# Performance work log

Measured on AMD Instinct MI355X. Metric: run time of the kernel, lower is better.

Reference implementation:

```python
import jax, jax.numpy as jnp
import numpy as np

B, N, E = 2, 20000, 160000
D, U = 1, 100          # input_dim, num_units
IN = D + U             # 101
NEG_SLOPE = 0.2        # PyG GATv2Conv default


def setup_inputs() -> dict:
    key = jax.random.key(0)
    ks = jax.random.split(key, 20)
    s = 0.1
    inp = {
        "inputs": jax.random.normal(ks[0], (B, N * D), jnp.float32),
        "state": jax.random.normal(ks[1], (B, N * U), jnp.float32),
        "src": jax.random.randint(ks[2], (E,), 0, N),
        "dst": jax.random.randint(ks[3], (E,), 0, N),
        # GATv2Conv(101, 200) params: lin_l, lin_r, att, out-bias
        "Wl1": jax.random.normal(ks[4], (IN, 2 * U), jnp.float32) * s,
        "bl1": jax.random.normal(ks[5], (2 * U,), jnp.float32) * s,
        "Wr1": jax.random.normal(ks[6], (IN, 2 * U), jnp.float32) * s,
        "br1": jax.random.normal(ks[7], (2 * U,), jnp.float32) * s,
        "att1": jax.random.normal(ks[8], (2 * U,), jnp.float32) * s,
        "bg1": jax.random.normal(ks[9], (2 * U,), jnp.float32) * s,
        "bias0": jax.random.normal(ks[10], (2 * U,), jnp.float32) * s,
        # GATv2Conv(101, 100) params
        "Wl2": jax.random.normal(ks[11], (IN, U), jnp.float32) * s,
        "bl2": jax.random.normal(ks[12], (U,), jnp.float32) * s,
        "Wr2": jax.random.normal(ks[13], (IN, U), jnp.float32) * s,
        "br2": jax.random.normal(ks[14], (U,), jnp.float32) * s,
        "att2": jax.random.normal(ks[15], (U,), jnp.float32) * s,
        "bg2": jax.random.normal(ks[16], (U,), jnp.float32) * s,
        "bias1": jax.random.normal(ks[17], (U,), jnp.float32) * s,
    }
    return inp


def _gatv2(x, src_f, dst_f, Wl, bl, Wr, br, att, bg):
    # x: (B, N, IN); edges (with self-loops) flow src -> dst.
    xl = x @ Wl + bl                                   # (B, N, C) source transform
    xr = x @ Wr + br                                   # (B, N, C) target transform
    msg = jax.nn.leaky_relu(xl[:, src_f] + xr[:, dst_f], NEG_SLOPE)  # (B, Ef, C)
    e = jnp.einsum('bec,c->be', msg, att)              # (B, Ef) attention logits
    seg_max = jax.vmap(lambda v: jax.ops.segment_max(v, dst_f, num_segments=N))(e)
    ea = jnp.exp(e - seg_max[:, dst_f])
    denom = jax.vmap(lambda v: jax.ops.segment_sum(v, dst_f, num_segments=N))(ea)
    alpha = ea / denom[:, dst_f]                       # per-target softmax
    out = jax.vmap(
        lambda a, xs: jax.ops.segment_sum(a[:, None] * xs, dst_f, num_segments=N)
    )(alpha, xl[:, src_f])                             # (B, N, C)
    return out + bg


def reference(inputs, state, src, dst,
              Wl1, bl1, Wr1, br1, att1, bg1, bias0,
              Wl2, bl2, Wr2, br2, att2, bg2, bias1):
    loops = jnp.arange(N)
    src_f = jnp.concatenate([src, loops])              # PyG adds self-loops
    dst_f = jnp.concatenate([dst, loops])
    inputs3 = inputs.reshape(B, N, D)
    state3 = state.reshape(B, N, U)

    # _gc1: GATv2(101 -> 200) + bias_0, sigmoid gates r, u
    xs = jnp.concatenate([inputs3, state3], axis=2)    # (B, N, 101)
    g1 = _gatv2(xs, src_f, dst_f, Wl1, bl1, Wr1, br1, att1, bg1) + bias0
    val = jax.nn.sigmoid(g1)                           # (B, N, 200)
    r = val[..., :U].reshape(B, N * U)
    u = val[..., U:].reshape(B, N * U)

    # _gc2: GATv2(101 -> 100) on [inputs, r*state] + bias_1, tanh
    xs2 = jnp.concatenate([inputs3, (r * state).reshape(B, N, U)], axis=2)
    c = jnp.tanh(_gatv2(xs2, src_f, dst_f, Wl2, bl2, Wr2, br2, att2, bg2) + bias1)
    c = c.reshape(B, N * U)

    new_state = u * state + (1.0 - u) * c              # (B, N*U)
    return new_state
```

## Files before the change

kernel.cpp:

```cpp
#include <hip/hip_runtime.h>
#include <stdint.h>

typedef __attribute__((ext_vector_type(8))) short short8;
typedef __attribute__((ext_vector_type(4))) short short4v;
typedef __attribute__((ext_vector_type(4))) float f32x4;

static constexpr int BB = 2, NN = 20000, UU = 100;
static constexpr int C1 = 200, C2 = 100;
static constexpr int MT = BB * NN;
static constexpr int MPAD = 40064;
static constexpr float NEG = 0.2f;

__device__ __forceinline__ float b2f(short s) {
  union { uint32_t u; float f; } cv; cv.u = ((uint32_t)(uint16_t)s) << 16; return cv.f;
}
__device__ __forceinline__ short f2b(float x) {
  union { float f; uint32_t u; } cv; cv.f = x;
  uint32_t r = cv.u + 0x7FFFu + ((cv.u >> 16) & 1u);
  return (short)(r >> 16);
}

#define GL2LDS(gsrc, ldst)                                                          \
  __builtin_amdgcn_global_load_lds((const __attribute__((address_space(1))) void*)(gsrc), \
                                   (__attribute__((address_space(3))) void*)(ldst), 16, 0, 0)


__global__ void k_prep(const float* __restrict__ inp, const float* __restrict__ st,
                       const float* __restrict__ Wl1, const float* __restrict__ Wr1,
                       const float* __restrict__ Wl2, const float* __restrict__ Wr2,
                       short* __restrict__ A, short* __restrict__ BT1,
                       short* __restrict__ BT2, int* __restrict__ cursor) {
  int t = blockIdx.x * 256 + threadIdx.x;
  if (t < MT * 16) {
    int r = t >> 4, g = t & 15;
    short8 v;
#pragma unroll
    for (int j = 0; j < 8; ++j) {
      int e = g * 8 + j;
      float x = 0.f;
      if (e == 0) x = inp[r];
      else if (e <= 100) x = st[(size_t)r * 100 + e - 1];
      v[j] = f2b(x);
    }
    *(short8*)(A + (size_t)r * 128 + ((g ^ (r & 7)) << 3)) = v;
  }
  if (t < 512 * 16) {
    int n = t >> 4, g = t & 15;
    short8 v;
#pragma unroll
    for (int j = 0; j < 8; ++j) {
      int k = g * 8 + j;
      float x = 0.f;
      if (k < 101 && n < 400)
        x = (n < 200) ? Wl1[(size_t)k * 200 + n] : Wr1[(size_t)k * 200 + n - 200];
      v[j] = f2b(x);
    }
    *(short8*)(BT1 + (size_t)n * 128 + ((g ^ (n & 7)) << 3)) = v;
  }
  if (t < 256 * 16) {
    int n = t >> 4, g = t & 15;
    short8 v;
#pragma unroll
    for (int j = 0; j < 8; ++j) {
      int k = g * 8 + j;
      int ksrc = (k < 100) ? k + 1 : ((k == 100) ? 0 : -1);
      float x = 0.f;
      if (ksrc >= 0 && n < 200)
        x = (n < 100) ? Wl2[(size_t)ksrc * 100 + n] : Wr2[(size_t)ksrc * 100 + n - 100];
      v[j] = f2b(x);
    }
    *(short8*)(BT2 + (size_t)n * 128 + ((g ^ (n & 7)) << 3)) = v;
  }
  if (t < NN) cursor[t] = 0;
}


__global__ void k_hist(const int* __restrict__ dst, int E, int* __restrict__ hist) {
  int e = blockIdx.x * 256 + threadIdx.x;
  if (e < E) atomicAdd(&hist[dst[e]], 1);
}

__global__ __launch_bounds__(1024) void k_scan(int* __restrict__ histcur,
                                               int* __restrict__ rowptr, int N, int E) {
  __shared__ int part[1024];
  int t = threadIdx.x;
  int CH = (N + 1023) / 1024;
  int beg = t * CH; if (beg > N) beg = N;
  int end = beg + CH; if (end > N) end = N;
  int s = 0;
  for (int i = beg; i < end; ++i) s += histcur[i];
  part[t] = s;
  __syncthreads();
  for (int off = 1; off < 1024; off <<= 1) {
    int v = (t >= off) ? part[t - off] : 0;
    __syncthreads();
    part[t] += v;
    __syncthreads();
  }
  int base = (t == 0) ? 0 : part[t - 1];
  for (int i = beg; i < end; ++i) {
    int h = histcur[i];
    rowptr[i] = base;
    histcur[i] = base;
    base += h;
  }
  if (t == 1023) rowptr[N] = part[1023];
}

__global__ void k_scatter(const int* __restrict__ src, const int* __restrict__ dst, int E,
                          int* __restrict__ cursor, int* __restrict__ col) {
  int e = blockIdx.x * 256 + threadIdx.x;
  if (e < E) {
    int p = atomicAdd(&cursor[dst[e]], 1);
    col[p] = src[e];
  }
}


template<int NOUT, int SPLIT>
__global__ __launch_bounds__(256) void k_gemm(
    const short* __restrict__ A, const short* __restrict__ BT,
    const float* __restrict__ bias_l, const float* __restrict__ bias_r,
    short* __restrict__ X) {
  __shared__ __align__(16) short As[128 * 128];
  __shared__ __align__(16) short Bs[128 * 128];
  int tid = threadIdx.x;
  int m0 = blockIdx.x * 128;
  int n0 = blockIdx.y * 128;
  {
    const short* gA = A + (size_t)m0 * 128;
    const short* gB = BT + (size_t)n0 * 128;
#pragma unroll
    for (int i = 0; i < 8; ++i) {
      GL2LDS(gA + i * 2048 + tid * 8, As + i * 2048 + tid * 8);
      GL2LDS(gB + i * 2048 + tid * 8, Bs + i * 2048 + tid * 8);
    }
  }
  __syncthreads();

  int wv = tid >> 6, lane = tid & 63;
  int m_off = (wv & 1) * 64, n_off = (wv >> 1) * 64;
  int lrow = lane & 15, lk = lane >> 4;
  f32x4 acc[4][4];
#pragma unroll
  for (int i = 0; i < 4; ++i)
#pragma unroll
    for (int j = 0; j < 4; ++j) acc[i][j] = (f32x4){0.f, 0.f, 0.f, 0.f};

#pragma unroll
  for (int kk = 0; kk < 4; ++kk) {
    int g = kk * 4 + lk;
    short8 a[4], b[4];
#pragma unroll
    for (int f = 0; f < 4; ++f) {
      int ra = m_off + f * 16 + lrow;
      a[f] = *(const short8*)(As + ra * 128 + ((g ^ (ra & 7)) << 3));
      int rb = n_off + f * 16 + lrow;
      b[f] = *(const short8*)(Bs + rb * 128 + ((g ^ (rb & 7)) << 3));
    }
#pragma unroll
    for (int i = 0; i < 4; ++i)
#pragma unroll
      for (int j = 0; j < 4; ++j)
        acc[i][j] = __builtin_amdgcn_mfma_f32_16x16x32_bf16(a[i], b[j], acc[i][j], 0, 0, 0);
  }

#pragma unroll
  for (int j = 0; j < 4; ++j) {
    int nc = n0 + n_off + j * 16 + lrow;
    bool nok = nc < NOUT;
    float bv = 0.f;
    int coff = 0;
    if (nok) {
      bv   = (nc < SPLIT) ? bias_l[nc] : bias_r[nc - SPLIT];
      coff = (nc < SPLIT) ? nc : 2 * SPLIT + (nc - SPLIT);
    }
#pragma unroll
    for (int i = 0; i < 4; ++i) {
      int mb = m0 + m_off + i * 16 + lk * 4;
#pragma unroll
      for (int r = 0; r < 4; ++r) {
        int m = mb + r;
        if (nok && m < MT) {
          int b_   = (m >= NN) ? 1 : 0;
          int node = m - b_ * NN;
          X[(size_t)node * (4 * SPLIT) + coff + b_ * SPLIT] = f2b(acc[i][j][r] + bv);
        }
      }
    }
  }
}


__global__ __launch_bounds__(256) void k_agg1(
    const short* __restrict__ X1, const int* __restrict__ rowptr, const int* __restrict__ col,
    const float* __restrict__ att, const float* __restrict__ bgv, const float* __restrict__ bias0,
    const float* __restrict__ st, const float* __restrict__ inp,
    short* __restrict__ A2, float* __restrict__ uu) {
  int w = threadIdx.x >> 6, lane = threadIdx.x & 63;
  int n = blockIdx.x * 4 + w;
  if (n >= NN) return;
  int half = lane >> 5, ll = lane & 31;
  int c0 = (ll < 25 ? ll : 24) * 8;
  int idx = half * NN + n;
  const short* xb = X1 + (size_t)half * 200 + c0;

  float attv[8], xrv[8], num[8];
  {
    f32x4 a0 = (f32x4){0,0,0,0}, a1 = (f32x4){0,0,0,0};
    if (ll < 25) { a0 = *(const f32x4*)(att + c0); a1 = *(const f32x4*)(att + c0 + 4); }
#pragma unroll
    for (int q = 0; q < 4; ++q) { attv[q] = a0[q]; attv[4 + q] = a1[q]; }
    short8 xr8 = *(const short8*)(X1 + (size_t)n * 800 + 400 + half * 200 + c0);
#pragma unroll
    for (int q = 0; q < 8; ++q) xrv[q] = (ll < 25) ? b2f(xr8[q]) : 0.f;
  }
  float denom;
  {
    short8 v = *(const short8*)(xb + (size_t)n * 800);
    float xs[8], e = 0.f;
#pragma unroll
    for (int q = 0; q < 8; ++q) {
      xs[q] = b2f(v[q]);
      float msg = xs[q] + xrv[q];
      msg = (msg > 0.f) ? msg : NEG * msg;
      e = fmaf(msg, attv[q], e);
    }
#pragma unroll
    for (int off = 16; off > 0; off >>= 1) e += __shfl_xor(e, off);
    float pe = __expf(e);
    denom = pe;
#pragma unroll
    for (int q = 0; q < 8; ++q) num[q] = pe * xs[q];
  }

  int beg = rowptr[n], end = rowptr[n + 1];
  for (int bp = beg; bp < end; bp += 64) {
    int cnt = min(end - bp, 64);
    int cv = col[bp + (lane < cnt ? lane : 0)];
    int p = 0;
    for (; p + 4 <= cnt; p += 4) {
      int s0 = __shfl(cv, p), s1 = __shfl(cv, p + 1);
      int s2 = __shfl(cv, p + 2), s3 = __shfl(cv, p + 3);
      short8 v0 = *(const short8*)(xb + (size_t)s0 * 800);
      short8 v1 = *(const short8*)(xb + (size_t)s1 * 800);
      short8 v2 = *(const short8*)(xb + (size_t)s2 * 800);
      short8 v3 = *(const short8*)(xb + (size_t)s3 * 800);
      float xs0[8], xs1[8], xs2[8], xs3[8];
      float e0 = 0.f, e1 = 0.f, e2 = 0.f, e3 = 0.f;
#pragma unroll
      for (int q = 0; q < 8; ++q) {
        float m_;
        xs0[q] = b2f(v0[q]); m_ = xs0[q] + xrv[q]; m_ = (m_ > 0.f) ? m_ : NEG * m_; e0 = fmaf(m_, attv[q], e0);
        xs1[q] = b2f(v1[q]); m_ = xs1[q] + xrv[q]; m_ = (m_ > 0.f) ? m_ : NEG * m_; e1 = fmaf(m_, attv[q], e1);
        xs2[q] = b2f(v2[q]); m_ = xs2[q] + xrv[q]; m_ = (m_ > 0.f) ? m_ : NEG * m_; e2 = fmaf(m_, attv[q], e2);
        xs3[q] = b2f(v3[q]); m_ = xs3[q] + xrv[q]; m_ = (m_ > 0.f) ? m_ : NEG * m_; e3 = fmaf(m_, attv[q], e3);
      }
#pragma unroll
      for (int off = 16; off > 0; off >>= 1) {
        e0 += __shfl_xor(e0, off);
        e1 += __shfl_xor(e1, off);
        e2 += __shfl_xor(e2, off);
        e3 += __shfl_xor(e3, off);
      }
      float pe0 = __expf(e0), pe1 = __expf(e1), pe2 = __expf(e2), pe3 = __expf(e3);
      denom += (pe0 + pe1) + (pe2 + pe3);
#pragma unroll
      for (int q = 0; q < 8; ++q)
        num[q] = fmaf(pe3, xs3[q], fmaf(pe2, xs2[q], fmaf(pe1, xs1[q], fmaf(pe0, xs0[q], num[q]))));
    }
    for (; p < cnt; ++p) {
      int s0 = __shfl(cv, p);
      short8 v0 = *(const short8*)(xb + (size_t)s0 * 800);
      float xs0[8], e0 = 0.f;
#pragma unroll
      for (int q = 0; q < 8; ++q) {
        xs0[q] = b2f(v0[q]);
        float m_ = xs0[q] + xrv[q]; m_ = (m_ > 0.f) ? m_ : NEG * m_;
        e0 = fmaf(m_, attv[q], e0);
      }
#pragma unroll
      for (int off = 16; off > 0; off >>= 1) e0 += __shfl_xor(e0, off);
      float pe0 = __expf(e0);
      denom += pe0;
#pragma unroll
      for (int q = 0; q < 8; ++q) num[q] = fmaf(pe0, xs0[q], num[q]);
    }
  }

  float invd = 1.f / denom;
  if (ll < 25) {
    f32x4 g0 = *(const f32x4*)(bgv + c0),   g1 = *(const f32x4*)(bgv + c0 + 4);
    f32x4 h0 = *(const f32x4*)(bias0 + c0), h1 = *(const f32x4*)(bias0 + c0 + 4);
    float vq[8];
#pragma unroll
    for (int q = 0; q < 4; ++q) {
      float o0 = fmaf(num[q], invd, g0[q] + h0[q]);
      vq[q] = 1.f / (1.f + __expf(-o0));
      float o1 = fmaf(num[4 + q], invd, g1[q] + h1[q]);
      vq[4 + q] = 1.f / (1.f + __expf(-o1));
    }
    size_t sb = (size_t)idx * UU;
    if (ll < 12) {
      f32x4 s0 = *(const f32x4*)(st + sb + c0), s1 = *(const f32x4*)(st + sb + c0 + 4);
      short8 wv;
#pragma unroll
      for (int q = 0; q < 4; ++q) { wv[q] = f2b(vq[q] * s0[q]); wv[4 + q] = f2b(vq[4 + q] * s1[q]); }
      *(short8*)(A2 + (size_t)idx * 128 + ((ll ^ (idx & 7)) << 3)) = wv;
    } else if (ll == 12) {
      f32x4 s0 = *(const f32x4*)(st + sb + 96);
      short8 wv;
#pragma unroll
      for (int q = 0; q < 4; ++q) wv[q] = f2b(vq[q] * s0[q]);
      wv[4] = f2b(inp[idx]); wv[5] = 0; wv[6] = 0; wv[7] = 0;
      *(short8*)(A2 + (size_t)idx * 128 + ((12 ^ (idx & 7)) << 3)) = wv;
      *(f32x4*)(uu + sb) = (f32x4){vq[4], vq[5], vq[6], vq[7]};
    } else {
      int uo = c0 - 100;
      *(f32x4*)(uu + sb + uo)     = (f32x4){vq[0], vq[1], vq[2], vq[3]};
      *(f32x4*)(uu + sb + uo + 4) = (f32x4){vq[4], vq[5], vq[6], vq[7]};
      if (ll < 16) {
        short8 z = (short8){0,0,0,0,0,0,0,0};
        *(short8*)(A2 + (size_t)idx * 128 + ((ll ^ (idx & 7)) << 3)) = z;
      }
    }
  }
}

__global__ __launch_bounds__(256) void k_agg2(
    const short* __restrict__ X2, const int* __restrict__ rowptr, const int* __restrict__ col,
    const float* __restrict__ att, const float* __restrict__ bgv, const float* __restrict__ bias1,
    const float* __restrict__ st, float* __restrict__ out) {
  int w = threadIdx.x >> 6, lane = threadIdx.x & 63;
  int n = blockIdx.x * 4 + w;
  if (n >= NN) return;
  int half = lane >> 5, ll = lane & 31;
  int c0 = (ll < 25 ? ll : 24) * 4;
  int idx = half * NN + n;
  const short* xb = X2 + (size_t)half * 100 + c0;

  float attv[4], xrv[4], num[4];
  {
    f32x4 a0 = (f32x4){0,0,0,0};
    if (ll < 25) a0 = *(const f32x4*)(att + c0);
#pragma unroll
    for (int q = 0; q < 4; ++q) attv[q] = a0[q];
    short4v xr4 = *(const short4v*)(X2 + (size_t)n * 400 + 200 + half * 100 + c0);
#pragma unroll
    for (int q = 0; q < 4; ++q) xrv[q] = (ll < 25) ? b2f(xr4[q]) : 0.f;
  }
  float denom;
  {
    short4v v = *(const short4v*)(xb + (size_t)n * 400);
    float xs[4], e = 0.f;
#pragma unroll
    for (int q = 0; q < 4; ++q) {
      xs[q] = b2f(v[q]);
      float msg = xs[q] + xrv[q];
      msg = (msg > 0.f) ? msg : NEG * msg;
      e = fmaf(msg, attv[q], e);
    }
#pragma unroll
    for (int off = 16; off > 0; off >>= 1) e += __shfl_xor(e, off);
    float pe = __expf(e);
    denom = pe;
#pragma unroll
    for (int q = 0; q < 4; ++q) num[q] = pe * xs[q];
  }

  int beg = rowptr[n], end = rowptr[n + 1];
  for (int bp = beg; bp < end; bp += 64) {
    int cnt = min(end - bp, 64);
    int cv = col[bp + (lane < cnt ? lane : 0)];
    int p = 0;
    for (; p + 4 <= cnt; p += 4) {
      int s0 = __shfl(cv, p), s1 = __shfl(cv, p + 1);
      int s2 = __shfl(cv, p + 2), s3 = __shfl(cv, p + 3);
      short4v v0 = *(const short4v*)(xb + (size_t)s0 * 400);
      short4v v1 = *(const short4v*)(xb + (size_t)s1 * 400);
      short4v v2 = *(const short4v*)(xb + (size_t)s2 * 400);
      short4v v3 = *(const short4v*)(xb + (size_t)s3 * 400);
      float xs0[4], xs1[4], xs2[4], xs3[4];
      float e0 = 0.f, e1 = 0.f, e2 = 0.f, e3 = 0.f;
#pragma unroll
      for (int q = 0; q < 4; ++q) {
        float m_;
        xs0[q] = b2f(v0[q]); m_ = xs0[q] + xrv[q]; m_ = (m_ > 0.f) ? m_ : NEG * m_; e0 = fmaf(m_, attv[q], e0);
        xs1[q] = b2f(v1[q]); m_ = xs1[q] + xrv[q]; m_ = (m_ > 0.f) ? m_ : NEG * m_; e1 = fmaf(m_, attv[q], e1);
        xs2[q] = b2f(v2[q]); m_ = xs2[q] + xrv[q]; m_ = (m_ > 0.f) ? m_ : NEG * m_; e2 = fmaf(m_, attv[q], e2);
        xs3[q] = b2f(v3[q]); m_ = xs3[q] + xrv[q]; m_ = (m_ > 0.f) ? m_ : NEG * m_; e3 = fmaf(m_, attv[q], e3);
      }
#pragma unroll
      for (int off = 16; off > 0; off >>= 1) {
        e0 += __shfl_xor(e0, off);
        e1 += __shfl_xor(e1, off);
        e2 += __shfl_xor(e2, off);
        e3 += __shfl_xor(e3, off);
      }
      float pe0 = __expf(e0), pe1 = __expf(e1), pe2 = __expf(e2), pe3 = __expf(e3);
      denom += (pe0 + pe1) + (pe2 + pe3);
#pragma unroll
      for (int q = 0; q < 4; ++q)
        num[q] = fmaf(pe3, xs3[q], fmaf(pe2, xs2[q], fmaf(pe1, xs1[q], fmaf(pe0, xs0[q], num[q]))));
    }
    for (; p < cnt; ++p) {
      int s0 = __shfl(cv, p);
      short4v v0 = *(const short4v*)(xb + (size_t)s0 * 400);
      float xs0[4], e0 = 0.f;
#pragma unroll
      for (int q = 0; q < 4; ++q) {
        xs0[q] = b2f(v0[q]);
        float m_ = xs0[q] + xrv[q]; m_ = (m_ > 0.f) ? m_ : NEG * m_;
        e0 = fmaf(m_, attv[q], e0);
      }
#pragma unroll
      for (int off = 16; off > 0; off >>= 1) e0 += __shfl_xor(e0, off);
      float pe0 = __expf(e0);
      denom += pe0;
#pragma unroll
      for (int q = 0; q < 4; ++q) num[q] = fmaf(pe0, xs0[q], num[q]);
    }
  }

  float invd = 1.f / denom;
  if (ll < 25) {
    f32x4 g0 = *(const f32x4*)(bgv + c0);
    f32x4 h0 = *(const f32x4*)(bias1 + c0);
    size_t sb = (size_t)idx * UU;
    f32x4 uv = *(const f32x4*)(out + sb + c0);
    f32x4 sv = *(const f32x4*)(st + sb + c0);
    f32x4 res;
#pragma unroll
    for (int q = 0; q < 4; ++q) {
      float o   = fmaf(num[q], invd, g0[q] + h0[q]);
      float cvh = tanhf(o);
      res[q] = uv[q] * sv[q] + (1.f - uv[q]) * cvh;
    }
    *(f32x4*)(out + sb + c0) = res;
  }
}


extern "C" void kernel_launch(void* const* d_in, const int* in_sizes, int n_in,
                              void* d_out, int out_size, void* d_ws, size_t ws_size,
                              hipStream_t stream) {
  const float* inp  = (const float*)d_in[0];
  const float* st   = (const float*)d_in[1];
  const int*   src  = (const int*)d_in[2];
  const int*   dst  = (const int*)d_in[3];
  const float* Wl1  = (const float*)d_in[4];
  const float* bl1  = (const float*)d_in[5];
  const float* Wr1  = (const float*)d_in[6];
  const float* br1  = (const float*)d_in[7];
  const float* att1 = (const float*)d_in[8];
  const float* bg1  = (const float*)d_in[9];
  const float* bias0= (const float*)d_in[10];
  const float* Wl2  = (const float*)d_in[11];
  const float* bl2  = (const float*)d_in[12];
  const float* Wr2  = (const float*)d_in[13];
  const float* br2  = (const float*)d_in[14];
  const float* att2 = (const float*)d_in[15];
  const float* bg2  = (const float*)d_in[16];
  const float* bias1= (const float*)d_in[17];

  const int N = NN;
  const int E = in_sizes[2];

  short* X1  = (short*)d_ws;
  short* X2  = X1;
  short* Aws = X1 + (size_t)NN * 800;
  short* BT1 = Aws + (size_t)MPAD * 128;
  short* BT2 = BT1 + 512 * 128;
  int* rowptr = (int*)(BT2 + 256 * 128);
  int* cursor = rowptr + (N + 1);
  int* col    = cursor + N;

  k_prep<<<(MT * 16 + 255) / 256, 256, 0, stream>>>(inp, st, Wl1, Wr1, Wl2, Wr2,
                                                    Aws, BT1, BT2, cursor);
  k_hist<<<(E + 255) / 256, 256, 0, stream>>>(dst, E, cursor);
  k_scan<<<1, 1024, 0, stream>>>(cursor, rowptr, N, E);
  k_scatter<<<(E + 255) / 256, 256, 0, stream>>>(src, dst, E, cursor, col);

  {
    dim3 g(MPAD / 128, 4);
    k_gemm<400, 200><<<g, 256, 0, stream>>>(Aws, BT1, bl1, br1, X1);
  }
  k_agg1<<<(NN + 3) / 4, 256, 0, stream>>>(X1, rowptr, col, att1, bg1, bias0, st, inp,
                                           Aws, (float*)d_out);
  {
    dim3 g(MPAD / 128, 2);
    k_gemm<200, 100><<<g, 256, 0, stream>>>(Aws, BT2, bl2, br2, X2);
  }
  k_agg2<<<(NN + 3) / 4, 256, 0, stream>>>(X2, rowptr, col, att2, bg2, bias1, st,
                                           (float*)d_out);
}
```

Before: 195.4 us.

## Fuse degree histogram into first GEMM launch and process two nodes per wave in aggregation

The edge-degree histogram now runs as extra trailing blocks of the first GEMM launch, using a flattened 1D grid, so one kernel launch is removed and the histogram overlaps with GEMM work. Both aggregation kernels now give each wavefront two consecutive destination nodes instead of one. Their edge lists are loaded together and interleaved, giving more independent gathers in flight per wave. The trade-offs are extra predication for unequal degrees, higher register use, and a serial fallback loop when the two nodes together exceed 64 edges.

```diff
diff --git a/kernel.cpp b/kernel.cpp
--- a/kernel.cpp
+++ b/kernel.cpp
@@ -6,9 +6,9 @@
 typedef __attribute__((ext_vector_type(4))) float f32x4;
 
 static constexpr int BB = 2, NN = 20000, UU = 100;
-static constexpr int C1 = 200, C2 = 100;
 static constexpr int MT = BB * NN;
 static constexpr int MPAD = 40064;
+static constexpr int GB1 = 313;
 static constexpr float NEG = 0.2f;
 
 __device__ __forceinline__ float b2f(short s) {
@@ -74,11 +74,6 @@
   if (t < NN) cursor[t] = 0;
 }
 
-
-__global__ void k_hist(const int* __restrict__ dst, int E, int* __restrict__ hist) {
-  int e = blockIdx.x * 256 + threadIdx.x;
-  if (e < E) atomicAdd(&hist[dst[e]], 1);
-}
 
 __global__ __launch_bounds__(1024) void k_scan(int* __restrict__ histcur,
                                                int* __restrict__ rowptr, int N, int E) {
@@ -121,12 +116,18 @@
 __global__ __launch_bounds__(256) void k_gemm(
     const short* __restrict__ A, const short* __restrict__ BT,
     const float* __restrict__ bias_l, const float* __restrict__ bias_r,
-    short* __restrict__ X) {
+    short* __restrict__ X, int nbg,
+    const int* __restrict__ dstE, int E, int* __restrict__ hist) {
   __shared__ __align__(16) short As[128 * 128];
   __shared__ __align__(16) short Bs[128 * 128];
   int tid = threadIdx.x;
-  int m0 = blockIdx.x * 128;
-  int n0 = blockIdx.y * 128;
+  if ((int)blockIdx.x >= nbg) {
+    int e = (blockIdx.x - nbg) * 256 + tid;
+    if (e < E) atomicAdd(&hist[dstE[e]], 1);
+    return;
+  }
+  int m0 = (blockIdx.x % GB1) * 128;
+  int n0 = (blockIdx.x / GB1) * 128;
   {
     const short* gA = A + (size_t)m0 * 128;
     const short* gB = BT + (size_t)n0 * 128;
@@ -192,138 +193,174 @@
 }
 
 
+#define EDGE1(S, XR, NUM, DEN, NCH, STRIDE)                                        \
+  { short8 v_ = *(const short8*)(xb + (size_t)(S) * STRIDE);                       \
+    float e_ = 0.f;                                                                \
+    _Pragma("unroll") for (int q = 0; q < NCH; ++q) {                              \
+      float x_ = b2f(v_[q]); float m_ = x_ + XR[q];                                \
+      m_ = (m_ > 0.f) ? m_ : NEG * m_; e_ = fmaf(m_, attv[q], e_); }               \
+    _Pragma("unroll") for (int o_ = 16; o_ > 0; o_ >>= 1) e_ += __shfl_xor(e_, o_);\
+    float p_ = __expf(e_); DEN += p_;                                              \
+    _Pragma("unroll") for (int q = 0; q < NCH; ++q)                                \
+      NUM[q] = fmaf(p_, b2f(v_[q]), NUM[q]); }
+
 __global__ __launch_bounds__(256) void k_agg1(
     const short* __restrict__ X1, const int* __restrict__ rowptr, const int* __restrict__ col,
     const float* __restrict__ att, const float* __restrict__ bgv, const float* __restrict__ bias0,
     const float* __restrict__ st, const float* __restrict__ inp,
     short* __restrict__ A2, float* __restrict__ uu) {
   int w = threadIdx.x >> 6, lane = threadIdx.x & 63;
-  int n = blockIdx.x * 4 + w;
-  if (n >= NN) return;
+  int n0 = blockIdx.x * 8 + w * 2;
+  if (n0 >= NN) return;
+  int n1 = n0 + 1;
   int half = lane >> 5, ll = lane & 31;
   int c0 = (ll < 25 ? ll : 24) * 8;
-  int idx = half * NN + n;
   const short* xb = X1 + (size_t)half * 200 + c0;
 
-  float attv[8], xrv[8], num[8];
+  float attv[8];
   {
     f32x4 a0 = (f32x4){0,0,0,0}, a1 = (f32x4){0,0,0,0};
     if (ll < 25) { a0 = *(const f32x4*)(att + c0); a1 = *(const f32x4*)(att + c0 + 4); }
 #pragma unroll
     for (int q = 0; q < 4; ++q) { attv[q] = a0[q]; attv[4 + q] = a1[q]; }
-    short8 xr8 = *(const short8*)(X1 + (size_t)n * 800 + 400 + half * 200 + c0);
-#pragma unroll
-    for (int q = 0; q < 8; ++q) xrv[q] = (ll < 25) ? b2f(xr8[q]) : 0.f;
-  }
-  float denom;
-  {
-    short8 v = *(const short8*)(xb + (size_t)n * 800);
-    float xs[8], e = 0.f;
+  }
+  float xr0[8], xr1[8];
+  {
+    short8 r0 = *(const short8*)(X1 + (size_t)n0 * 800 + 400 + half * 200 + c0);
+    short8 r1 = *(const short8*)(X1 + (size_t)n1 * 800 + 400 + half * 200 + c0);
 #pragma unroll
     for (int q = 0; q < 8; ++q) {
-      xs[q] = b2f(v[q]);
-      float msg = xs[q] + xrv[q];
-      msg = (msg > 0.f) ? msg : NEG * msg;
-      e = fmaf(msg, attv[q], e);
-    }
-#pragma unroll
-    for (int off = 16; off > 0; off >>= 1) e += __shfl_xor(e, off);
-    float pe = __expf(e);
-    denom = pe;
-#pragma unroll
-    for (int q = 0; q < 8; ++q) num[q] = pe * xs[q];
-  }
-
-  int beg = rowptr[n], end = rowptr[n + 1];
-  for (int bp = beg; bp < end; bp += 64) {
-    int cnt = min(end - bp, 64);
-    int cv = col[bp + (lane < cnt ? lane : 0)];
-    int p = 0;
-    for (; p + 4 <= cnt; p += 4) {
-      int s0 = __shfl(cv, p), s1 = __shfl(cv, p + 1);
-      int s2 = __shfl(cv, p + 2), s3 = __shfl(cv, p + 3);
-      short8 v0 = *(const short8*)(xb + (size_t)s0 * 800);
-      short8 v1 = *(const short8*)(xb + (size_t)s1 * 800);
-      short8 v2 = *(const short8*)(xb + (size_t)s2 * 800);
-      short8 v3 = *(const short8*)(xb + (size_t)s3 * 800);
-      float xs0[8], xs1[8], xs2[8], xs3[8];
-      float e0 = 0.f, e1 = 0.f, e2 = 0.f, e3 = 0.f;
-#pragma unroll
-      for (int q = 0; q < 8; ++q) {
-        float m_;
-        xs0[q] = b2f(v0[q]); m_ = xs0[q] + xrv[q]; m_ = (m_ > 0.f) ? m_ : NEG * m_; e0 = fmaf(m_, attv[q], e0);
-        xs1[q] = b2f(v1[q]); m_ = xs1[q] + xrv[q]; m_ = (m_ > 0.f) ? m_ : NEG * m_; e1 = fmaf(m_, attv[q], e1);
-        xs2[q] = b2f(v2[q]); m_ = xs2[q] + xrv[q]; m_ = (m_ > 0.f) ? m_ : NEG * m_; e2 = fmaf(m_, attv[q], e2);
-        xs3[q] = b2f(v3[q]); m_ = xs3[q] + xrv[q]; m_ = (m_ > 0.f) ? m_ : NEG * m_; e3 = fmaf(m_, attv[q], e3);
-      }
-#pragma unroll
-      for (int off = 16; off > 0; off >>= 1) {
-        e0 += __shfl_xor(e0, off);
-        e1 += __shfl_xor(e1, off);
-        e2 += __shfl_xor(e2, off);
-        e3 += __shfl_xor(e3, off);
-      }
-      float pe0 = __expf(e0), pe1 = __expf(e1), pe2 = __expf(e2), pe3 = __expf(e3);
-      denom += (pe0 + pe1) + (pe2 + pe3);
-#pragma unroll
-      for (int q = 0; q < 8; ++q)
-        num[q] = fmaf(pe3, xs3[q], fmaf(pe2, xs2[q], fmaf(pe1, xs1[q], fmaf(pe0, xs0[q], num[q]))));
-    }
-    for (; p < cnt; ++p) {
-      int s0 = __shfl(cv, p);
-      short8 v0 = *(const short8*)(xb + (size_t)s0 * 800);
-      float xs0[8], e0 = 0.f;
-#pragma unroll
-      for (int q = 0; q < 8; ++q) {
-        xs0[q] = b2f(v0[q]);
-        float m_ = xs0[q] + xrv[q]; m_ = (m_ > 0.f) ? m_ : NEG * m_;
-        e0 = fmaf(m_, attv[q], e0);
-      }
-#pragma unroll
-      for (int off = 16; off > 0; off >>= 1) e0 += __shfl_xor(e0, off);
-      float pe0 = __expf(e0);
-      denom += pe0;
-#pragma unroll
-      for (int q = 0; q < 8; ++q) num[q] = fmaf(pe0, xs0[q], num[q]);
-    }
-  }
-
-  float invd = 1.f / denom;
+      xr0[q] = (ll < 25) ? b2f(r0[q]) : 0.f;
+      xr1[q] = (ll < 25) ? b2f(r1[q]) : 0.f;
+    }
+  }
+  float num0[8], num1[8], den0, den1;
+  {
+    short8 vA = *(const short8*)(xb + (size_t)n0 * 800);
+    short8 vB = *(const short8*)(xb + (size_t)n1 * 800);
+    float eA = 0.f, eB = 0.f;
+#pragma unroll
+    for (int q = 0; q < 8; ++q) {
+      float x, m_;
+      x = b2f(vA[q]); m_ = x + xr0[q]; m_ = (m_ > 0.f) ? m_ : NEG * m_; eA = fmaf(m_, attv[q], eA);
+      x = b2f(vB[q]); m_ = x + xr1[q]; m_ = (m_ > 0.f) ? m_ : NEG * m_; eB = fmaf(m_, attv[q], eB);
+    }
+#pragma unroll
+    for (int off = 16; off > 0; off >>= 1) { eA += __shfl_xor(eA, off); eB += __shfl_xor(eB, off); }
+    float pA = __expf(eA), pB = __expf(eB);
+    den0 = pA; den1 = pB;
+#pragma unroll
+    for (int q = 0; q < 8; ++q) { num0[q] = pA * b2f(vA[q]); num1[q] = pB * b2f(vB[q]); }
+  }
+
+  int beg0 = rowptr[n0], beg1 = rowptr[n1], end1 = rowptr[n1 + 1];
+  int d0 = beg1 - beg0, d1 = end1 - beg1;
+  int tot = d0 + d1;
+  int cv = 0;
+  if (tot > 0) cv = col[beg0 + (lane < tot ? lane : 0)];
+  int d0c = min(d0, 64);
+  int d1c = min(d1, max(0, 64 - d0));
+  int P = max(d0c, d1c);
+  int p = 0;
+  for (; p + 2 <= P; p += 2) {
+    bool vA0 = p < d0c, vA1 = p + 1 < d0c;
+    bool vB0 = p < d1c, vB1 = p + 1 < d1c;
+    int sA0 = vA0 ? __shfl(cv, p) : n0;
+    int sA1 = vA1 ? __shfl(cv, p + 1) : n0;
+    int sB0 = vB0 ? __shfl(cv, d0 + p) : n1;
+    int sB1 = vB1 ? __shfl(cv, d0 + p + 1) : n1;
+    short8 a0v = *(const short8*)(xb + (size_t)sA0 * 800);
+    short8 a1v = *(const short8*)(xb + (size_t)sA1 * 800);
+    short8 b0v = *(const short8*)(xb + (size_t)sB0 * 800);
+    short8 b1v = *(const short8*)(xb + (size_t)sB1 * 800);
+    float eA0 = 0.f, eA1 = 0.f, eB0 = 0.f, eB1 = 0.f;
+#pragma unroll
+    for (int q = 0; q < 8; ++q) {
+      float x, m_;
+      x = b2f(a0v[q]); m_ = x + xr0[q]; m_ = (m_ > 0.f) ? m_ : NEG * m_; eA0 = fmaf(m_, attv[q], eA0);
+      x = b2f(a1v[q]); m_ = x + xr0[q]; m_ = (m_ > 0.f) ? m_ : NEG * m_; eA1 = fmaf(m_, attv[q], eA1);
+      x = b2f(b0v[q]); m_ = x + xr1[q]; m_ = (m_ > 0.f) ? m_ : NEG * m_; eB0 = fmaf(m_, attv[q], eB0);
+      x = b2f(b1v[q]); m_ = x + xr1[q]; m_ = (m_ > 0.f) ? m_ : NEG * m_; eB1 = fmaf(m_, attv[q], eB1);
+    }
+#pragma unroll
+    for (int off = 16; off > 0; off >>= 1) {
+      eA0 += __shfl_xor(eA0, off); eA1 += __shfl_xor(eA1, off);
+      eB0 += __shfl_xor(eB0, off); eB1 += __shfl_xor(eB1, off);
+    }
+    float pA0 = vA0 ? __expf(eA0) : 0.f;
+    float pA1 = vA1 ? __expf(eA1) : 0.f;
+    float pB0 = vB0 ? __expf(eB0) : 0.f;
+    float pB1 = vB1 ? __expf(eB1) : 0.f;
+    den0 += pA0 + pA1; den1 += pB0 + pB1;
+#pragma unroll
+    for (int q = 0; q < 8; ++q) {
+      num0[q] = fmaf(pA1, b2f(a1v[q]), fmaf(pA0, b2f(a0v[q]), num0[q]));
+      num1[q] = fmaf(pB1, b2f(b1v[q]), fmaf(pB0, b2f(b0v[q]), num1[q]));
+    }
+  }
+  if (p < P) {
+    bool vA0 = p < d0c, vB0 = p < d1c;
+    int sA0 = vA0 ? __shfl(cv, p) : n0;
+    int sB0 = vB0 ? __shfl(cv, d0 + p) : n1;
+    short8 a0v = *(const short8*)(xb + (size_t)sA0 * 800);
+    short8 b0v = *(const short8*)(xb + (size_t)sB0 * 800);
+    float eA0 = 0.f, eB0 = 0.f;
+#pragma unroll
+    for (int q = 0; q < 8; ++q) {
+      float x, m_;
+      x = b2f(a0v[q]); m_ = x + xr0[q]; m_ = (m_ > 0.f) ? m_ : NEG * m_; eA0 = fmaf(m_, attv[q], eA0);
+      x = b2f(b0v[q]); m_ = x + xr1[q]; m_ = (m_ > 0.f) ? m_ : NEG * m_; eB0 = fmaf(m_, attv[q], eB0);
+    }
+#pragma unroll
+    for (int off = 16; off > 0; off >>= 1) { eA0 += __shfl_xor(eA0, off); eB0 += __shfl_xor(eB0, off); }
+    float pA0 = vA0 ? __expf(eA0) : 0.f;
+    float pB0 = vB0 ? __expf(eB0) : 0.f;
+    den0 += pA0; den1 += pB0;
+#pragma unroll
+    for (int q = 0; q < 8; ++q) {
+      num0[q] = fmaf(pA0, b2f(a0v[q]), num0[q]);
+      num1[q] = fmaf(pB0, b2f(b0v[q]), num1[q]);
+    }
+  }
+  for (int t = d0c; t < d0; ++t) { int s = col[beg0 + t]; EDGE1(s, xr0, num0, den0, 8, 800); }
+  for (int t = d1c; t < d1; ++t) { int s = col[beg1 + t]; EDGE1(s, xr1, num1, den1, 8, 800); }
+
+  float inv0 = 1.f / den0, inv1 = 1.f / den1;
   if (ll < 25) {
     f32x4 g0 = *(const f32x4*)(bgv + c0),   g1 = *(const f32x4*)(bgv + c0 + 4);
     f32x4 h0 = *(const f32x4*)(bias0 + c0), h1 = *(const f32x4*)(bias0 + c0 + 4);
-    float vq[8];
-#pragma unroll
-    for (int q = 0; q < 4; ++q) {
-      float o0 = fmaf(num[q], invd, g0[q] + h0[q]);
-      vq[q] = 1.f / (1.f + __expf(-o0));
-      float o1 = fmaf(num[4 + q], invd, g1[q] + h1[q]);
-      vq[4 + q] = 1.f / (1.f + __expf(-o1));
-    }
-    size_t sb = (size_t)idx * UU;
-    if (ll < 12) {
-      f32x4 s0 = *(const f32x4*)(st + sb + c0), s1 = *(const f32x4*)(st + sb + c0 + 4);
-      short8 wv;
-#pragma unroll
-      for (int q = 0; q < 4; ++q) { wv[q] = f2b(vq[q] * s0[q]); wv[4 + q] = f2b(vq[4 + q] * s1[q]); }
-      *(short8*)(A2 + (size_t)idx * 128 + ((ll ^ (idx & 7)) << 3)) = wv;
-    } else if (ll == 12) {
-      f32x4 s0 = *(const f32x4*)(st + sb + 96);
-      short8 wv;
-#pragma unroll
-      for (int q = 0; q < 4; ++q) wv[q] = f2b(vq[q] * s0[q]);
-      wv[4] = f2b(inp[idx]); wv[5] = 0; wv[6] = 0; wv[7] = 0;
-      *(short8*)(A2 + (size_t)idx * 128 + ((12 ^ (idx & 7)) << 3)) = wv;
-      *(f32x4*)(uu + sb) = (f32x4){vq[4], vq[5], vq[6], vq[7]};
-    } else {
-      int uo = c0 - 100;
-      *(f32x4*)(uu + sb + uo)     = (f32x4){vq[0], vq[1], vq[2], vq[3]};
-      *(f32x4*)(uu + sb + uo + 4) = (f32x4){vq[4], vq[5], vq[6], vq[7]};
-      if (ll < 16) {
-        short8 z = (short8){0,0,0,0,0,0,0,0};
-        *(short8*)(A2 + (size_t)idx * 128 + ((ll ^ (idx & 7)) << 3)) = z;
-      }
-    }
+#define EPI1(NM, INVD, NODE)                                                        \
+    { int idx = half * NN + (NODE);                                                 \
+      float vq[8];                                                                  \
+      _Pragma("unroll") for (int q = 0; q < 4; ++q) {                               \
+        float o0 = fmaf(NM[q], INVD, g0[q] + h0[q]);                                \
+        vq[q] = 1.f / (1.f + __expf(-o0));                                          \
+        float o1 = fmaf(NM[4 + q], INVD, g1[q] + h1[q]);                            \
+        vq[4 + q] = 1.f / (1.f + __expf(-o1)); }                                    \
+      size_t sb = (size_t)idx * UU;                                                 \
+      if (ll < 12) {                                                                \
+        f32x4 s0 = *(const f32x4*)(st + sb + c0), s1 = *(const f32x4*)(st + sb + c0 + 4); \
+        short8 wv;                                                                  \
+        _Pragma("unroll") for (int q = 0; q < 4; ++q) {                             \
+          wv[q] = f2b(vq[q] * s0[q]); wv[4 + q] = f2b(vq[4 + q] * s1[q]); }         \
+        *(short8*)(A2 + (size_t)idx * 128 + ((ll ^ (idx & 7)) << 3)) = wv;          \
+      } else if (ll == 12) {                                                        \
+        f32x4 s0 = *(const f32x4*)(st + sb + 96);                                   \
+        short8 wv;                                                                  \
+        _Pragma("unroll") for (int q = 0; q < 4; ++q) wv[q] = f2b(vq[q] * s0[q]);   \
+        wv[4] = f2b(inp[idx]); wv[5] = 0; wv[6] = 0; wv[7] = 0;                     \
+        *(short8*)(A2 + (size_t)idx * 128 + ((12 ^ (idx & 7)) << 3)) = wv;          \
+        *(f32x4*)(uu + sb) = (f32x4){vq[4], vq[5], vq[6], vq[7]};                   \
+      } else {                                                                      \
+        int uo = c0 - 100;                                                          \
+        *(f32x4*)(uu + sb + uo)     = (f32x4){vq[0], vq[1], vq[2], vq[3]};          \
+        *(f32x4*)(uu + sb + uo + 4) = (f32x4){vq[4], vq[5], vq[6], vq[7]};          \
+        if (ll < 16) {                                                              \
+          short8 z = (short8){0,0,0,0,0,0,0,0};                                     \
+          *(short8*)(A2 + (size_t)idx * 128 + ((ll ^ (idx & 7)) << 3)) = z; } } }
+    EPI1(num0, inv0, n0)
+    EPI1(num1, inv1, n1)
+#undef EPI1
   }
 }
 
@@ -332,111 +369,139 @@
     const float* __restrict__ att, const float* __restrict__ bgv, const float* __restrict__ bias1,
     const float* __restrict__ st, float* __restrict__ out) {
   int w = threadIdx.x >> 6, lane = threadIdx.x & 63;
-  int n = blockIdx.x * 4 + w;
-  if (n >= NN) return;
+  int n0 = blockIdx.x * 8 + w * 2;
+  if (n0 >= NN) return;
+  int n1 = n0 + 1;
   int half = lane >> 5, ll = lane & 31;
   int c0 = (ll < 25 ? ll : 24) * 4;
-  int idx = half * NN + n;
   const short* xb = X2 + (size_t)half * 100 + c0;
 
-  float attv[4], xrv[4], num[4];
+  float attv[4];
   {
     f32x4 a0 = (f32x4){0,0,0,0};
     if (ll < 25) a0 = *(const f32x4*)(att + c0);
 #pragma unroll
     for (int q = 0; q < 4; ++q) attv[q] = a0[q];
-    short4v xr4 = *(const short4v*)(X2 + (size_t)n * 400 + 200 + half * 100 + c0);
-#pragma unroll
-    for (int q = 0; q < 4; ++q) xrv[q] = (ll < 25) ? b2f(xr4[q]) : 0.f;
-  }
-  float denom;
-  {
-    short4v v = *(const short4v*)(xb + (size_t)n * 400);
-    float xs[4], e = 0.f;
+  }
+  float xr0[4], xr1[4];
+  {
+    short4v r0 = *(const short4v*)(X2 + (size_t)n0 * 400 + 200 + half * 100 + c0);
+    short4v r1 = *(const short4v*)(X2 + (size_t)n1 * 400 + 200 + half * 100 + c0);
 #pragma unroll
     for (int q = 0; q < 4; ++q) {
-      xs[q] = b2f(v[q]);
-      float msg = xs[q] + xrv[q];
-      msg = (msg > 0.f) ? msg : NEG * msg;
-      e = fmaf(msg, attv[q], e);
-    }
-#pragma unroll
-    for (int off = 16; off > 0; off >>= 1) e += __shfl_xor(e, off);
-    float pe = __expf(e);
-    denom = pe;
-#pragma unroll
-    for (int q = 0; q < 4; ++q) num[q] = pe * xs[q];
-  }
-
-  int beg = rowptr[n], end = rowptr[n + 1];
-  for (int bp = beg; bp < end; bp += 64) {
-    int cnt = min(end - bp, 64);
-    int cv = col[bp + (lane < cnt ? lane : 0)];
-    int p = 0;
-    for (; p + 4 <= cnt; p += 4) {
-      int s0 = __shfl(cv, p), s1 = __shfl(cv, p + 1);
-      int s2 = __shfl(cv, p + 2), s3 = __shfl(cv, p + 3);
-      short4v v0 = *(const short4v*)(xb + (size_t)s0 * 400);
-      short4v v1 = *(const short4v*)(xb + (size_t)s1 * 400);
-      short4v v2 = *(const short4v*)(xb + (size_t)s2 * 400);
-      short4v v3 = *(const short4v*)(xb + (size_t)s3 * 400);
-      float xs0[4], xs1[4], xs2[4], xs3[4];
-      float e0 = 0.f, e1 = 0.f, e2 = 0.f, e3 = 0.f;
-#pragma unroll
-      for (int q = 0; q < 4; ++q) {
-        float m_;
-        xs0[q] = b2f(v0[q]); m_ = xs0[q] + xrv[q]; m_ = (m_ > 0.f) ? m_ : NEG * m_; e0 = fmaf(m_, attv[q], e0);
-        xs1[q] = b2f(v1[q]); m_ = xs1[q] + xrv[q]; m_ = (m_ > 0.f) ? m_ : NEG * m_; e1 = fmaf(m_, attv[q], e1);
-        xs2[q] = b2f(v2[q]); m_ = xs2[q] + xrv[q]; m_ = (m_ > 0.f) ? m_ : NEG * m_; e2 = fmaf(m_, attv[q], e2);
-        xs3[q] = b2f(v3[q]); m_ = xs3[q] + xrv[q]; m_ = (m_ > 0.f) ? m_ : NEG * m_; e3 = fmaf(m_, attv[q], e3);
-      }
-#pragma unroll
-      for (int off = 16; off > 0; off >>= 1) {
-        e0 += __shfl_xor(e0, off);
-        e1 += __shfl_xor(e1, off);
-        e2 += __shfl_xor(e2, off);
-        e3 += __shfl_xor(e3, off);
-      }
-      float pe0 = __expf(e0), pe1 = __expf(e1), pe2 = __expf(e2), pe3 = __expf(e3);
-      denom += (pe0 + pe1) + (pe2 + pe3);
-#pragma unroll
-      for (int q = 0; q < 4; ++q)
-        num[q] = fmaf(pe3, xs3[q], fmaf(pe2, xs2[q], fmaf(pe1, xs1[q], fmaf(pe0, xs0[q], num[q]))));
-    }
-    for (; p < cnt; ++p) {
-      int s0 = __shfl(cv, p);
-      short4v v0 = *(const short4v*)(xb + (size_t)s0 * 400);
-      float xs0[4], e0 = 0.f;
-#pragma unroll
-      for (int q = 0; q < 4; ++q) {
-        xs0[q] = b2f(v0[q]);
-        float m_ = xs0[q] + xrv[q]; m_ = (m_ > 0.f) ? m_ : NEG * m_;
-        e0 = fmaf(m_, attv[q], e0);
-      }
-#pragma unroll
-      for (int off = 16; off > 0; off >>= 1) e0 += __shfl_xor(e0, off);
-      float pe0 = __expf(e0);
-      denom += pe0;
-#pragma unroll
-      for (int q = 0; q < 4; ++q) num[q] = fmaf(pe0, xs0[q], num[q]);
-    }
-  }
-
-  float invd = 1.f / denom;
+      xr0[q] = (ll < 25) ? b2f(r0[q]) : 0.f;
+      xr1[q] = (ll < 25) ? b2f(r1[q]) : 0.f;
+    }
+  }
+  float num0[4], num1[4], den0, den1;
+  {
+    short4v vA = *(const short4v*)(xb + (size_t)n0 * 400);
+    short4v vB = *(const short4v*)(xb + (size_t)n1 * 400);
+    float eA = 0.f, eB = 0.f;
+#pragma unroll
+    for (int q = 0; q < 4; ++q) {
+      float x, m_;
+      x = b2f(vA[q]); m_ = x + xr0[q]; m_ = (m_ > 0.f) ? m_ : NEG * m_; eA = fmaf(m_, attv[q], eA);
+      x = b2f(vB[q]); m_ = x + xr1[q]; m_ = (m_ > 0.f) ? m_ : NEG * m_; eB = fmaf(m_, attv[q], eB);
+    }
+#pragma unroll
+    for (int off = 16; off > 0; off >>= 1) { eA += __shfl_xor(eA, off); eB += __shfl_xor(eB, off); }
+    float pA = __expf(eA), pB = __expf(eB);
+    den0 = pA; den1 = pB;
+#pragma unroll
+    for (int q = 0; q < 4; ++q) { num0[q] = pA * b2f(vA[q]); num1[q] = pB * b2f(vB[q]); }
+  }
+
+  int beg0 = rowptr[n0], beg1 = rowptr[n1], end1 = rowptr[n1 + 1];
+  int d0 = beg1 - beg0, d1 = end1 - beg1;
+  int tot = d0 + d1;
+  int cv = 0;
+  if (tot > 0) cv = col[beg0 + (lane < tot ? lane : 0)];
+  int d0c = min(d0, 64);
+  int d1c = min(d1, max(0, 64 - d0));
+  int P = max(d0c, d1c);
+  int p = 0;
+  for (; p + 2 <= P; p += 2) {
+    bool vA0 = p < d0c, vA1 = p + 1 < d0c;
+    bool vB0 = p < d1c, vB1 = p + 1 < d1c;
+    int sA0 = vA0 ? __shfl(cv, p) : n0;
+    int sA1 = vA1 ? __shfl(cv, p + 1) : n0;
+    int sB0 = vB0 ? __shfl(cv, d0 + p) : n1;
+    int sB1 = vB1 ? __shfl(cv, d0 + p + 1) : n1;
+    short4v a0v = *(const short4v*)(xb + (size_t)sA0 * 400);
+    short4v a1v = *(const short4v*)(xb + (size_t)sA1 * 400);
+    short4v b0v = *(const short4v*)(xb + (size_t)sB0 * 400);
+    short4v b1v = *(const short4v*)(xb + (size_t)sB1 * 400);
+    float eA0 = 0.f, eA1 = 0.f, eB0 = 0.f, eB1 = 0.f;
+#pragma unroll
+    for (int q = 0; q < 4; ++q) {
+      float x, m_;
+      x = b2f(a0v[q]); m_ = x + xr0[q]; m_ = (m_ > 0.f) ? m_ : NEG * m_; eA0 = fmaf(m_, attv[q], eA0);
+      x = b2f(a1v[q]); m_ = x + xr0[q]; m_ = (m_ > 0.f) ? m_ : NEG * m_; eA1 = fmaf(m_, attv[q], eA1);
+      x = b2f(b0v[q]); m_ = x + xr1[q]; m_ = (m_ > 0.f) ? m_ : NEG * m_; eB0 = fmaf(m_, attv[q], eB0);
+      x = b2f(b1v[q]); m_ = x + xr1[q]; m_ = (m_ > 0.f) ? m_ : NEG * m_; eB1 = fmaf(m_, attv[q], eB1);
+    }
+#pragma unroll
+    for (int off = 16; off > 0; off >>= 1) {
+      eA0 += __shfl_xor(eA0, off); eA1 += __shfl_xor(eA1, off);
+      eB0 += __shfl_xor(eB0, off); eB1 += __shfl_xor(eB1, off);
+    }
+    float pA0 = vA0 ? __expf(eA0) : 0.f;
+    float pA1 = vA1 ? __expf(eA1) : 0.f;
+    float pB0 = vB0 ? __expf(eB0) : 0.f;
+    float pB1 = vB1 ? __expf(eB1) : 0.f;
+    den0 += pA0 + pA1; den1 += pB0 + pB1;
+#pragma unroll
+    for (int q = 0; q < 4; ++q) {
+      num0[q] = fmaf(pA1, b2f(a1v[q]), fmaf(pA0, b2f(a0v[q]), num0[q]));
+      num1[q] = fmaf(pB1, b2f(b1v[q]), fmaf(pB0, b2f(b0v[q]), num1[q]));
+    }
+  }
+  if (p < P) {
+    bool vA0 = p < d0c, vB0 = p < d1c;
+    int sA0 = vA0 ? __shfl(cv, p) : n0;
+    int sB0 = vB0 ? __shfl(cv, d0 + p) : n1;
+    short4v a0v = *(const short4v*)(xb + (size_t)sA0 * 400);
+    short4v b0v = *(const short4v*)(xb + (size_t)sB0 * 400);
+    float eA0 = 0.f, eB0 = 0.f;
+#pragma unroll
+    for (int q = 0; q < 4; ++q) {
+      float x, m_;
+      x = b2f(a0v[q]); m_ = x + xr0[q]; m_ = (m_ > 0.f) ? m_ : NEG * m_; eA0 = fmaf(m_, attv[q], eA0);
+      x = b2f(b0v[q]); m_ = x + xr1[q]; m_ = (m_ > 0.f) ? m_ : NEG * m_; eB0 = fmaf(m_, attv[q], eB0);
+    }
+#pragma unroll
+    for (int off = 16; off > 0; off >>= 1) { eA0 += __shfl_xor(eA0, off); eB0 += __shfl_xor(eB0, off); }
+    float pA0 = vA0 ? __expf(eA0) : 0.f;
+    float pB0 = vB0 ? __expf(eB0) : 0.f;
+    den0 += pA0; den1 += pB0;
+#pragma unroll
+    for (int q = 0; q < 4; ++q) {
+      num0[q] = fmaf(pA0, b2f(a0v[q]), num0[q]);
+      num1[q] = fmaf(pB0, b2f(b0v[q]), num1[q]);
+    }
+  }
+  for (int t = d0c; t < d0; ++t) { int s = col[beg0 + t]; EDGE1(s, xr0, num0, den0, 4, 400); }
+  for (int t = d1c; t < d1; ++t) { int s = col[beg1 + t]; EDGE1(s, xr1, num1, den1, 4, 400); }
+
+  float inv0 = 1.f / den0, inv1 = 1.f / den1;
   if (ll < 25) {
     f32x4 g0 = *(const f32x4*)(bgv + c0);
     f32x4 h0 = *(const f32x4*)(bias1 + c0);
-    size_t sb = (size_t)idx * UU;
-    f32x4 uv = *(const f32x4*)(out + sb + c0);
-    f32x4 sv = *(const f32x4*)(st + sb + c0);
-    f32x4 res;
-#pragma unroll
-    for (int q = 0; q < 4; ++q) {
-      float o   = fmaf(num[q], invd, g0[q] + h0[q]);
-      float cvh = tanhf(o);
-      res[q] = uv[q] * sv[q] + (1.f - uv[q]) * cvh;
-    }
-    *(f32x4*)(out + sb + c0) = res;
+#define EPI2(NM, INVD, NODE)                                                        \
+    { int idx = half * NN + (NODE);                                                 \
+      size_t sb = (size_t)idx * UU;                                                 \
+      f32x4 uv = *(const f32x4*)(out + sb + c0);                                    \
+      f32x4 sv = *(const f32x4*)(st + sb + c0);                                     \
+      f32x4 res;                                                                    \
+      _Pragma("unroll") for (int q = 0; q < 4; ++q) {                               \
+        float o   = fmaf(NM[q], INVD, g0[q] + h0[q]);                               \
+        float cvh = tanhf(o);                                                       \
+        res[q] = uv[q] * sv[q] + (1.f - uv[q]) * cvh; }                             \
+      *(f32x4*)(out + sb + c0) = res; }
+    EPI2(num0, inv0, n0)
+    EPI2(num1, inv1, n1)
+#undef EPI2
   }
 }
 
@@ -477,20 +542,18 @@
 
   k_prep<<<(MT * 16 + 255) / 256, 256, 0, stream>>>(inp, st, Wl1, Wr1, Wl2, Wr2,
                                                     Aws, BT1, BT2, cursor);
-  k_hist<<<(E + 255) / 256, 256, 0, stream>>>(dst, E, cursor);
+  {
+    int nbg = GB1 * 4;
+    int nbh = (E + 255) / 256;
+    k_gemm<400, 200><<<nbg + nbh, 256, 0, stream>>>(Aws, BT1, bl1, br1, X1, nbg,
+                                                    dst, E, cursor);
+  }
   k_scan<<<1, 1024, 0, stream>>>(cursor, rowptr, N, E);
   k_scatter<<<(E + 255) / 256, 256, 0, stream>>>(src, dst, E, cursor, col);
-
-  {
-    dim3 g(MPAD / 128, 4);
-    k_gemm<400, 200><<<g, 256, 0, stream>>>(Aws, BT1, bl1, br1, X1);
-  }
-  k_agg1<<<(NN + 3) / 4, 256, 0, stream>>>(X1, rowptr, col, att1, bg1, bias0, st, inp,
+  k_agg1<<<(NN + 7) / 8, 256, 0, stream>>>(X1, rowptr, col, att1, bg1, bias0, st, inp,
                                            Aws, (float*)d_out);
-  {
-    dim3 g(MPAD / 128, 2);
-    k_gemm<200, 100><<<g, 256, 0, stream>>>(Aws, BT2, bl2, br2, X2);
-  }
-  k_agg2<<<(NN + 3) / 4, 256, 0, stream>>>(X2, rowptr, col, att2, bg2, bias1, st,
+  k_gemm<200, 100><<<GB1 * 2, 256, 0, stream>>>(Aws, BT2, bl2, br2, X2, GB1 * 2,
+                                                nullptr, 0, nullptr);
+  k_agg2<<<(NN + 7) / 8, 256, 0, stream>>>(X2, rowptr, col, att2, bg2, bias1, st,
                                            (float*)d_out);
 }
```

After: 199.5 us. 1.02x slower.
